# Kernel tuning notes

Measured on AMD Instinct MI355X. Metric: run time of the kernel, lower is better.

## Reference

```python
import jax, jax.numpy as jnp
import numpy as np

N_HEAD = 16          # word_dim=1024 -> head_dim=64
SCALE = True         # scale_attentions=True
NEG_INF = -1.0e9


def setup_inputs() -> dict:
    key = jax.random.key(0)
    k0, k1, k2 = jax.random.split(key, 3)
    B, S, D = 8, 1024, 1024
    x = jax.random.normal(k0, (B, S, D), dtype=jnp.float32)
    W_qkv = jax.random.normal(k1, (D, 3 * D), dtype=jnp.float32) * 0.02
    b_qkv = jnp.zeros((3 * D,), dtype=jnp.float32)
    W_out = jax.random.normal(k2, (D, D), dtype=jnp.float32) * 0.02
    b_out = jnp.zeros((D,), dtype=jnp.float32)
    return {"x": x, "W_qkv": W_qkv, "b_qkv": b_qkv, "W_out": W_out, "b_out": b_out}


def reference(x, W_qkv, b_qkv, W_out, b_out):
    B, S, D = x.shape
    dh = D // N_HEAD
    # fused QKV pointwise (kernel_size=1 conv == linear) projection
    qkv = x @ W_qkv + b_qkv                      # [B, S, 3D]
    q, k, v = jnp.split(qkv, 3, axis=-1)         # each [B, S, D]

    def heads(t):
        return t.reshape(B, S, N_HEAD, dh).transpose(0, 2, 1, 3)  # [B, H, S, dh]

    q, k, v = heads(q), heads(k), heads(v)
    scores = jnp.einsum('bhqd,bhkd->bhqk', q, k)  # [B, H, S, S]
    if SCALE:
        scores = scores / jnp.sqrt(jnp.asarray(dh, scores.dtype))
    # custom causal masking: multiplicative mask + additive large-negative term
    mask = jnp.tril(jnp.ones((S, S), dtype=scores.dtype))  # [S, S]
    scores = scores * mask + NEG_INF * (1.0 - mask)
    w = jax.nn.softmax(scores, axis=-1)          # attn_dropout is identity in eval
    out = jnp.einsum('bhqk,bhkd->bhqd', w, v)    # [B, H, S, dh]
    out = out.transpose(0, 2, 1, 3).reshape(B, S, D)  # regroup heads
    return out @ W_out + b_out                   # output_dropout is identity in eval
```

## Files before the change

kernel.cpp:

```cpp
#include <hip/hip_runtime.h>
#include <hip/hip_bf16.h>

typedef __attribute__((ext_vector_type(8))) short short8;
typedef __attribute__((ext_vector_type(4))) float f32x4;
typedef __attribute__((ext_vector_type(4))) unsigned short us4;

#define GK 1024

#define EXP2F(x) __builtin_amdgcn_exp2f(x)

__device__ __forceinline__ unsigned short f2bf(float f) {
  unsigned int u = __float_as_uint(f);
  u += 0x7fffu + ((u >> 16) & 1u);
  return (unsigned short)(u >> 16);
}

__device__ __forceinline__ void gload16(const void* g, void* lds_base ) {
  __builtin_amdgcn_global_load_lds(
      (const __attribute__((address_space(1))) unsigned int*)g,
      (__attribute__((address_space(3))) unsigned int*)lds_base, 16, 0, 0);
}

__global__ void cast4_f32_bf16(const float* __restrict__ in, unsigned short* __restrict__ out, int n) {
  int i = (blockIdx.x * 256 + threadIdx.x) * 4;
  if (i >= n) return;
  float4 v = *(const float4*)(in + i);
  us4 o = { f2bf(v.x), f2bf(v.y), f2bf(v.z), f2bf(v.w) };
  *(us4*)(out + i) = o;
}

__global__ void transcast(const float* __restrict__ in, unsigned short* __restrict__ out, int K, int N) {
  __shared__ float t[32][33];
  int n0 = blockIdx.x * 32, k0 = blockIdx.y * 32;
  int tx = threadIdx.x, ty = threadIdx.y;
#pragma unroll
  for (int i = 0; i < 4; ++i)
    t[ty * 4 + i][tx] = in[(size_t)(k0 + ty * 4 + i) * N + n0 + tx];
  __syncthreads();
#pragma unroll
  for (int i = 0; i < 4; ++i)
    out[(size_t)(n0 + ty * 4 + i) * K + k0 + tx] = f2bf(t[tx][ty * 4 + i]);
}

template <int OUT_BF16>
__global__ __launch_bounds__(256) void gemm_nt(
    const unsigned short* __restrict__ A,
    const unsigned short* __restrict__ Bt,
    const float* __restrict__ bias,
    void* __restrict__ C, int M, int N)
{
  __shared__ __align__(16) unsigned short Asm[128 * 64];
  __shared__ __align__(16) unsigned short Bsm[128 * 64];

  int flat = blockIdx.y * gridDim.x + blockIdx.x;
  int span = 8 * gridDim.y;
  int stripe = flat / span;
  int r = flat - stripe * span;
  int bm = stripe * 8 + (r & 7);
  int bn = r >> 3;

  int t = threadIdx.x, w = t >> 6, l = t & 63;
  int wm = w >> 1, wn = w & 1;
  int g = l >> 4, ln = l & 15;

  const unsigned short* Ablk = A + (size_t)(bm * 128) * GK;
  const unsigned short* Bblk = Bt + (size_t)(bn * 128) * GK;

  f32x4 acc[4][4] = {};

  int srow_in = l >> 3;
  int scol = (((l & 7) ^ (l >> 3)) * 8);
  int swA = ln & 7;

  for (int kt = 0; kt < GK / 64; ++kt) {
    __syncthreads();
    int k0 = kt * 64 + scol;
#pragma unroll
    for (int j = 0; j < 4; ++j) {
      int chunk = w + 4 * j;
      int row = chunk * 8 + srow_in;
      gload16(Ablk + (size_t)row * GK + k0, Asm + chunk * 512);
      gload16(Bblk + (size_t)row * GK + k0, Bsm + chunk * 512);
    }
    __syncthreads();

#pragma unroll
    for (int ks = 0; ks < 2; ++ks) {
      int pc = ((ks * 4 + g) ^ swA) * 8;
      short8 af[4], bf[4];
#pragma unroll
      for (int mt = 0; mt < 4; ++mt) {
        int row = wm * 64 + ln + mt * 16;
        af[mt] = *(const short8*)(Asm + row * 64 + pc);
      }
#pragma unroll
      for (int nt = 0; nt < 4; ++nt) {
        int row = wn * 64 + ln + nt * 16;
        bf[nt] = *(const short8*)(Bsm + row * 64 + pc);
      }
#pragma unroll
      for (int mt = 0; mt < 4; ++mt)
#pragma unroll
        for (int nt = 0; nt < 4; ++nt)
          acc[mt][nt] = __builtin_amdgcn_mfma_f32_16x16x32_bf16(af[mt], bf[nt], acc[mt][nt], 0, 0, 0);
    }
  }

  int rowb = bm * 128 + wm * 64 + (g << 2);
  int colb = bn * 128 + wn * 64 + ln;
#pragma unroll
  for (int nt = 0; nt < 4; ++nt) {
    int col = colb + nt * 16;
    float bv = bias[col];
#pragma unroll
    for (int mt = 0; mt < 4; ++mt) {
      int row = rowb + mt * 16;
#pragma unroll
      for (int r2 = 0; r2 < 4; ++r2) {
        float v = acc[mt][nt][r2] + bv;
        if (OUT_BF16) ((unsigned short*)C)[(size_t)(row + r2) * N + col] = f2bf(v);
        else          ((float*)C)[(size_t)(row + r2) * N + col] = v;
      }
    }
  }
}

__global__ void transpose_v(const unsigned short* __restrict__ qkvb, unsigned short* __restrict__ Vt) {
  __shared__ __align__(16) unsigned short tile[64][72];
  int blk = blockIdx.x;
  int st = blk & 15, bh = blk >> 4, h = bh & 15, b = bh >> 4;
  int t = threadIdx.x;
  int srow = t >> 2, c0 = (t & 3) * 2;

  const unsigned short* src = qkvb + (size_t)(b * 1024 + st * 64 + srow) * 3072 + 2048 + h * 64;
#pragma unroll
  for (int j = 0; j < 2; ++j)
    *(short8*)(&tile[srow][(c0 + j) * 8]) = *(const short8*)(src + (c0 + j) * 8);
  __syncthreads();

  int d = t >> 2;
  unsigned short* dst = Vt + (size_t)(bh * 64 + d) * 1024 + st * 64;
#pragma unroll
  for (int j = 0; j < 2; ++j) {
    int s0 = (c0 + j) * 8;
    short8 v;
#pragma unroll
    for (int i = 0; i < 8; ++i) v[i] = tile[s0 + i][d];
    *(short8*)(dst + s0) = v;
  }
}

__global__ __launch_bounds__(256) void attn(
    const unsigned short* __restrict__ qkv,
    const unsigned short* __restrict__ Vt,
    unsigned short* __restrict__ Ob)
{
  __shared__ __align__(16) unsigned short Ksm[2][64 * 64];
  __shared__ __align__(16) unsigned short Vsm[2][64 * 64];
  __shared__ __align__(16) unsigned short Psm[4][16 * 64];

  const float C1 = 0.18033688011112042f;

  int t = threadIdx.x, w = t >> 6, l = t & 63;
  int g = l >> 4, ln = l & 15;
  int blk = blockIdx.x;
  int bh = blk & 127, pb = blk >> 7;
  int h = bh & 15, b = bh >> 4;

  const unsigned short* Kg = qkv + (size_t)(b * 1024) * 3072 + 1024 + h * 64;
  const unsigned short* Vg = Vt + (size_t)(bh * 64) * 1024;
  unsigned short* P = Psm[w];

  int jrow = l >> 3;
  int jc   = l & 7;
  int cur = 0;

  auto stage = [&](int buf, int kt) {
#pragma unroll
    for (int jj = 0; jj < 2; ++jj) {
      int j = 2 * w + jj;
      int row = j * 8 + jrow;
      int sc = jc ^ (row & 7);
      gload16(Kg + (size_t)(kt * 64 + row) * 3072 + sc * 8, (unsigned short*)Ksm[buf] + j * 512);
      gload16(Vg + (size_t)row * 1024 + kt * 64 + sc * 8,   (unsigned short*)Vsm[buf] + j * 512);
    }
  };

  int pwbase = ln * 64 + (g & 1) * 4;

#pragma unroll
  for (int half = 0; half < 2; ++half) {
    int qt = half ? (15 - pb) : pb;

    const unsigned short* qbase =
        qkv + (size_t)(b * 1024 + qt * 64 + w * 16 + ln) * 3072 + h * 64 + g * 8;
    short8 qf0 = *(const short8*)(qbase);
    short8 qf1 = *(const short8*)(qbase + 32);

    f32x4 acc_o[4] = {};
    float m2 = -1.0e30f, lsum = 0.f;

    stage(cur, 0);
    __syncthreads();

    for (int kt = 0; kt <= qt; ++kt) {
      bool last = (kt == qt);
      if (!last) stage(cur ^ 1, kt + 1);

      const unsigned short* Kb = Ksm[cur];
      f32x4 s[4] = {};
#pragma unroll
      for (int nt = 0; nt < 4; ++nt) {
        int krow = nt * 16 + ln;
        short8 k0 = *(const short8*)(Kb + krow * 64 + ((g ^ (krow & 7)) * 8));
        short8 k1 = *(const short8*)(Kb + krow * 64 + (((4 + g) ^ (krow & 7)) * 8));
        s[nt] = __builtin_amdgcn_mfma_f32_16x16x32_bf16(k0, qf0, s[nt], 0, 0, 0);
        s[nt] = __builtin_amdgcn_mfma_f32_16x16x32_bf16(k1, qf1, s[nt], 0, 0, 0);
      }

      if (last) {
        int qrow = w * 16 + ln;
#pragma unroll
        for (int nt = 0; nt < 4; ++nt)
#pragma unroll
          for (int r = 0; r < 4; ++r)
            if (nt * 16 + g * 4 + r > qrow) s[nt][r] = -1.0e9f;
      }

      float mx0 = fmaxf(fmaxf(s[0][0], s[0][1]), fmaxf(s[0][2], s[0][3]));
      float mx1 = fmaxf(fmaxf(s[1][0], s[1][1]), fmaxf(s[1][2], s[1][3]));
      float mx2 = fmaxf(fmaxf(s[2][0], s[2][1]), fmaxf(s[2][2], s[2][3]));
      float mx3 = fmaxf(fmaxf(s[3][0], s[3][1]), fmaxf(s[3][2], s[3][3]));
      float mraw = fmaxf(fmaxf(mx0, mx1), fmaxf(mx2, mx3));
      mraw = fmaxf(mraw, __shfl_xor(mraw, 16));
      mraw = fmaxf(mraw, __shfl_xor(mraw, 32));
      float m2cand = mraw * C1;

      if (!__all(m2cand <= m2)) {
        float m2new = fmaxf(m2, m2cand);
        float corr = EXP2F(m2 - m2new);
        m2 = m2new;
        lsum *= corr;
#pragma unroll
        for (int nt = 0; nt < 4; ++nt)
#pragma unroll
          for (int r = 0; r < 4; ++r) acc_o[nt][r] *= corr;
      }

      float rs = 0.f;
#pragma unroll
      for (int nt = 0; nt < 4; ++nt)
#pragma unroll
        for (int r = 0; r < 4; ++r) {
          float p = EXP2F(fmaf(s[nt][r], C1, -m2));
          s[nt][r] = p;
          rs += p;
        }
      rs += __shfl_xor(rs, 16);
      rs += __shfl_xor(rs, 32);
      lsum += rs;

#pragma unroll
      for (int nt = 0; nt < 4; ++nt) {
        us4 pk = { f2bf(s[nt][0]), f2bf(s[nt][1]), f2bf(s[nt][2]), f2bf(s[nt][3]) };
        *(us4*)(P + pwbase + (((nt * 2 + (g >> 1)) ^ (ln & 7)) * 8)) = pk;
      }
      short8 pa0 = *(const short8*)(P + ln * 64 + ((g ^ (ln & 7)) * 8));
      short8 pa1 = *(const short8*)(P + ln * 64 + (((4 + g) ^ (ln & 7)) * 8));

      const unsigned short* Vb = Vsm[cur];
#pragma unroll
      for (int nt = 0; nt < 4; ++nt) {
        int vrow = nt * 16 + ln;
        short8 vb0 = *(const short8*)(Vb + vrow * 64 + ((g ^ (vrow & 7)) * 8));
        short8 vb1 = *(const short8*)(Vb + vrow * 64 + (((4 + g) ^ (vrow & 7)) * 8));
        acc_o[nt] = __builtin_amdgcn_mfma_f32_16x16x32_bf16(vb0, pa0, acc_o[nt], 0, 0, 0);
        acc_o[nt] = __builtin_amdgcn_mfma_f32_16x16x32_bf16(vb1, pa1, acc_o[nt], 0, 0, 0);
      }

      __syncthreads();
      cur ^= 1;
    }

    float inv = 1.0f / lsum;
    size_t orow = (size_t)(b * 1024 + qt * 64 + w * 16 + ln);
#pragma unroll
    for (int nt = 0; nt < 4; ++nt) {
      us4 o = { f2bf(acc_o[nt][0] * inv), f2bf(acc_o[nt][1] * inv),
                f2bf(acc_o[nt][2] * inv), f2bf(acc_o[nt][3] * inv) };
      *(us4*)(Ob + orow * 1024 + h * 64 + nt * 16 + g * 4) = o;
    }
  }
}

extern "C" void kernel_launch(void* const* d_in, const int* in_sizes, int n_in,
                              void* d_out, int out_size, void* d_ws, size_t ws_size,
                              hipStream_t stream) {
  (void)in_sizes; (void)n_in; (void)out_size; (void)ws_size;
  const float* x    = (const float*)d_in[0];
  const float* Wqkv = (const float*)d_in[1];
  const float* bqkv = (const float*)d_in[2];
  const float* Wout = (const float*)d_in[3];
  const float* bout = (const float*)d_in[4];

  char* ws = (char*)d_ws;
  unsigned short* xb   = (unsigned short*)(ws);
  unsigned short* Wt1  = (unsigned short*)(ws + 16777216);
  unsigned short* Wt2  = (unsigned short*)(ws + 23068672);
  unsigned short* qkvb = (unsigned short*)(ws + 25165824);
  unsigned short* Vt   = (unsigned short*)(ws + 75497472);
  unsigned short* Ob   = (unsigned short*)(ws + 92274688);

  cast4_f32_bf16<<<8192, 256, 0, stream>>>(x, xb, 8192 * 1024);
  transcast<<<dim3(96, 32), dim3(32, 8), 0, stream>>>(Wqkv, Wt1, 1024, 3072);
  transcast<<<dim3(32, 32), dim3(32, 8), 0, stream>>>(Wout, Wt2, 1024, 1024);

  gemm_nt<1><<<dim3(64, 24), 256, 0, stream>>>(xb, Wt1, bqkv, qkvb, 8192, 3072);
  transpose_v<<<2048, 256, 0, stream>>>(qkvb, Vt);
  attn<<<1024, 256, 0, stream>>>(qkvb, Vt, Ob);
  gemm_nt<0><<<dim3(64, 8), 256, 0, stream>>>(Ob, Wt2, bout, (float*)d_out, 8192, 1024);
}
```

Before: 238.3 us.

## Replace QKV GEMM with 256x256-tile 8-wave double-buffered ping-pong kernel

Adds a new QKV projection GEMM that uses 256x256 block tiles, 512 threads (8 waves) and double-buffered LDS. Global-to-LDS loads for the next K tile are interleaved with MFMA phases, using explicit waitcnt and barrier scheduling plus setprio around the MFMA blocks. The larger tile is meant to raise arithmetic intensity, and the schedule is meant to hide load latency behind compute. In exchange it uses 128 KB of LDS and many registers, and the grid shrinks to 384 blocks, which may hurt occupancy or tail balance.

Measured after the change: 251.8 us. +5.6%, slower.

```diff
diff --git a/kernel.cpp b/kernel.cpp
--- a/kernel.cpp
+++ b/kernel.cpp
@@ -8,6 +8,12 @@
 #define GK 1024
 
 #define EXP2F(x) __builtin_amdgcn_exp2f(x)
+
+#define BARRIER() __builtin_amdgcn_s_barrier()
+#define LGKM0()  do { asm volatile("s_waitcnt lgkmcnt(0)" ::: "memory"); \
+                      __builtin_amdgcn_sched_barrier(0); } while (0)
+#define VMC4()   asm volatile("s_waitcnt vmcnt(4)" ::: "memory")
+#define VMC0()   asm volatile("s_waitcnt vmcnt(0)" ::: "memory")
 
 __device__ __forceinline__ unsigned short f2bf(float f) {
   unsigned int u = __float_as_uint(f);
@@ -40,6 +46,146 @@
 #pragma unroll
   for (int i = 0; i < 4; ++i)
     out[(size_t)(n0 + ty * 4 + i) * K + k0 + tx] = f2bf(t[tx][ty * 4 + i]);
+}
+
+__global__ __launch_bounds__(512, 2) void gemm8p(
+    const unsigned short* __restrict__ A,
+    const unsigned short* __restrict__ Bt,
+    const float* __restrict__ bias,
+    unsigned short* __restrict__ C, int M, int N)
+{
+  __shared__ __align__(16) unsigned short Asm[2][256 * 64];
+  __shared__ __align__(16) unsigned short Bsm[2][256 * 64];
+
+  int t = threadIdx.x, w = t >> 6, l = t & 63;
+  int wm = w >> 2, wn = w & 3;
+  int g = l >> 4, ln = l & 15, sw = ln & 7;
+
+  int flat = blockIdx.y * gridDim.x + blockIdx.x;
+  int span = 8 * gridDim.y;
+  int stripe = flat / span;
+  int rr = flat - stripe * span;
+  int bm = stripe * 8 + (rr & 7);
+  int bn = rr >> 3;
+
+  const unsigned short* Ablk = A + (size_t)(bm * 256) * GK;
+  const unsigned short* Bblk = Bt + (size_t)(bn * 256) * GK;
+
+  f32x4 acc[8][4] = {};
+  short8 a[2][8];
+  short8 bq[2][2];
+
+  int rin = l >> 3;
+  int scol = ((l & 7) ^ (l >> 3)) * 8;
+
+#define SA(BUF, KT, HALF) do {                                                     \
+    const unsigned short* _s = Ablk + (size_t)((HALF) * 128) * GK + (KT) * 64;     \
+    _Pragma("unroll")                                                              \
+    for (int _j = 0; _j < 2; ++_j) {                                               \
+      int _cg = 2 * w + _j;                                                        \
+      gload16(_s + (size_t)(_cg * 8 + rin) * GK + scol,                            \
+              &Asm[BUF][(HALF) * 8192 + _cg * 512]);                               \
+    } } while (0)
+#define SBst(BUF, KT, HALF) do {                                                   \
+    const unsigned short* _s = Bblk + (size_t)((HALF) * 128) * GK + (KT) * 64;     \
+    _Pragma("unroll")                                                              \
+    for (int _j = 0; _j < 2; ++_j) {                                               \
+      int _cg = 2 * w + _j;                                                        \
+      gload16(_s + (size_t)(_cg * 8 + rin) * GK + scol,                            \
+              &Bsm[BUF][(HALF) * 8192 + _cg * 512]);                               \
+    } } while (0)
+
+#define RDA(BUF, MS) do {                                                          \
+    _Pragma("unroll")                                                              \
+    for (int _mf = 0; _mf < 4; ++_mf) {                                            \
+      int _row = wm * 128 + ((MS) * 4 + _mf) * 16 + ln;                            \
+      _Pragma("unroll")                                                            \
+      for (int _ks = 0; _ks < 2; ++_ks)                                            \
+        a[_ks][(MS) * 4 + _mf] =                                                   \
+          *(const short8*)(&Asm[BUF][_row * 64 + (((_ks * 4 + g) ^ sw) * 8)]);     \
+    } } while (0)
+#define RDB(BUF, NS) do {                                                          \
+    _Pragma("unroll")                                                              \
+    for (int _nf = 0; _nf < 2; ++_nf) {                                            \
+      int _row = wn * 64 + ((NS) * 2 + _nf) * 16 + ln;                             \
+      _Pragma("unroll")                                                            \
+      for (int _ks = 0; _ks < 2; ++_ks)                                            \
+        bq[_ks][_nf] =                                                             \
+          *(const short8*)(&Bsm[BUF][_row * 64 + (((_ks * 4 + g) ^ sw) * 8)]);     \
+    } } while (0)
+
+#define MMA(MS, NS) do {                                                           \
+    __builtin_amdgcn_s_setprio(1);                                                 \
+    _Pragma("unroll")                                                              \
+    for (int _mf = 0; _mf < 4; ++_mf)                                              \
+      _Pragma("unroll")                                                            \
+      for (int _nf = 0; _nf < 2; ++_nf) {                                          \
+        int _am = (MS) * 4 + _mf, _an = (NS) * 2 + _nf;                            \
+        acc[_am][_an] = __builtin_amdgcn_mfma_f32_16x16x32_bf16(                   \
+            a[0][_am], bq[0][_nf], acc[_am][_an], 0, 0, 0);                        \
+        acc[_am][_an] = __builtin_amdgcn_mfma_f32_16x16x32_bf16(                   \
+            a[1][_am], bq[1][_nf], acc[_am][_an], 0, 0, 0);                        \
+      }                                                                            \
+    __builtin_amdgcn_s_setprio(0); } while (0)
+
+#define GEMM_ITER(T0, STEADY) do {                                                 \
+                                                                           \
+    RDA(0, 0); RDB(0, 0); SBst(1, (T0) + 1, 0);                                    \
+    BARRIER(); LGKM0(); MMA(0, 0); BARRIER();                                      \
+                                                                           \
+    RDA(0, 1); SBst(1, (T0) + 1, 1);                                               \
+    BARRIER(); LGKM0(); MMA(1, 0); BARRIER();                                      \
+                                                                           \
+    RDB(0, 1); if (STEADY) SA(0, (T0) + 2, 0);                                     \
+    BARRIER(); LGKM0(); MMA(1, 1); BARRIER();                                      \
+                                                                           \
+    if (STEADY) { SA(0, (T0) + 2, 1); VMC4(); } else { VMC0(); }                   \
+    BARRIER(); MMA(0, 1); BARRIER();                                               \
+                                                                           \
+    RDA(1, 0); RDB(1, 0); if (STEADY) SBst(0, (T0) + 2, 0);                        \
+    BARRIER(); LGKM0(); MMA(0, 0); BARRIER();                                      \
+                                                                           \
+    RDA(1, 1); if (STEADY) SBst(0, (T0) + 2, 1);                                   \
+    BARRIER(); LGKM0(); MMA(1, 0); BARRIER();                                      \
+                                                                           \
+    RDB(1, 1); if (STEADY) SA(1, (T0) + 3, 0);                                     \
+    BARRIER(); LGKM0(); MMA(1, 1); BARRIER();                                      \
+                                                                           \
+    if (STEADY) { SA(1, (T0) + 3, 1); VMC4(); BARRIER(); }                         \
+    MMA(0, 1);                                                                     \
+    if (STEADY) BARRIER();                                                         \
+  } while (0)
+
+  SA(0, 0, 0); SA(0, 0, 1); SBst(0, 0, 0); SBst(0, 0, 1);
+  SA(1, 1, 0); SA(1, 1, 1);
+  VMC4();
+  BARRIER();
+
+  for (int j = 0; j < 7; ++j) {
+    GEMM_ITER(2 * j, 1);
+  }
+  GEMM_ITER(14, 0);
+
+  int rowb = bm * 256 + wm * 128 + g * 4;
+  int colb = bn * 256 + wn * 64 + ln;
+#pragma unroll
+  for (int nf = 0; nf < 4; ++nf) {
+    int col = colb + nf * 16;
+    float bv = bias[col];
+#pragma unroll
+    for (int mf = 0; mf < 8; ++mf) {
+      int row = rowb + mf * 16;
+#pragma unroll
+      for (int r2 = 0; r2 < 4; ++r2)
+        C[(size_t)(row + r2) * N + col] = f2bf(acc[mf][nf][r2] + bv);
+    }
+  }
+#undef SA
+#undef SBst
+#undef RDA
+#undef RDB
+#undef MMA
+#undef GEMM_ITER
 }
 
 template <int OUT_BF16>
@@ -315,7 +461,7 @@
   transcast<<<dim3(96, 32), dim3(32, 8), 0, stream>>>(Wqkv, Wt1, 1024, 3072);
   transcast<<<dim3(32, 32), dim3(32, 8), 0, stream>>>(Wout, Wt2, 1024, 1024);
 
-  gemm_nt<1><<<dim3(64, 24), 256, 0, stream>>>(xb, Wt1, bqkv, qkvb, 8192, 3072);
+  gemm8p<<<dim3(32, 12), 512, 0, stream>>>(xb, Wt1, bqkv, qkvb, 8192, 3072);
   transpose_v<<<2048, 256, 0, stream>>>(qkvb, Vt);
   attn<<<1024, 256, 0, stream>>>(qkvb, Vt, Ob);
   gemm_nt<0><<<dim3(64, 8), 256, 0, stream>>>(Ob, Wt2, bout, (float*)d_out, 8192, 1024);
```
